# Kernel optimization log

Measured on AMD Instinct MI355X. Metric: run time of the kernel, lower is better.

The kernel has to match this reference:

```python
import jax, jax.numpy as jnp
import numpy as np
from jax import lax

B, C, V, T = 8, 256, 96, 96
C8, C2 = C // 8, C // 2


def _conv3(x, w):
    # 3x3, stride 1, pad 1, no bias (the repo's misnamed 'conv1x1')
    return lax.conv_general_dilated(x, w, (1, 1), [(1, 1), (1, 1)],
                                    dimension_numbers=("NCHW", "OIHW", "NCHW"))


def _conv1(x, w, b):
    # true 1x1 conv with bias (cAttn q/k/v)
    y = lax.conv_general_dilated(x, w, (1, 1), [(0, 0), (0, 0)],
                                 dimension_numbers=("NCHW", "OIHW", "NCHW"))
    return y + b[None, :, None, None]


def setup_inputs() -> dict:
    key = jax.random.key(0)
    ks = jax.random.split(key, 20)
    s = 0.02
    d = {
        "x": jax.random.normal(ks[0], (B, C, V, T), jnp.float32),
        # vAttn (3x3 convs, no bias)
        "v_wq": jax.random.normal(ks[1], (C8, C, 3, 3), jnp.float32) * s,
        "v_wk": jax.random.normal(ks[2], (C8, C, 3, 3), jnp.float32) * s,
        "v_wv": jax.random.normal(ks[3], (C2, C, 3, 3), jnp.float32) * s,
        "v_wo": jax.random.normal(ks[4], (C, C2, 3, 3), jnp.float32) * s,
        "v_sigma": jax.random.normal(ks[5], (1,), jnp.float32),
        # tAttn
        "t_wq": jax.random.normal(ks[6], (C8, C, 3, 3), jnp.float32) * s,
        "t_wk": jax.random.normal(ks[7], (C8, C, 3, 3), jnp.float32) * s,
        "t_wv": jax.random.normal(ks[8], (C2, C, 3, 3), jnp.float32) * s,
        "t_wo": jax.random.normal(ks[9], (C, C2, 3, 3), jnp.float32) * s,
        "t_sigma": jax.random.normal(ks[10], (1,), jnp.float32),
        # cAttn (1x1 convs with bias for q/k/v, 3x3 for output proj)
        "c_wq": jax.random.normal(ks[11], (C, C, 1, 1), jnp.float32) * s,
        "c_bq": jax.random.normal(ks[12], (C,), jnp.float32) * s,
        "c_wk": jax.random.normal(ks[13], (C, C, 1, 1), jnp.float32) * s,
        "c_bk": jax.random.normal(ks[14], (C,), jnp.float32) * s,
        "c_wv": jax.random.normal(ks[15], (C, C, 1, 1), jnp.float32) * s,
        "c_bv": jax.random.normal(ks[16], (C,), jnp.float32) * s,
        "c_wo": jax.random.normal(ks[17], (C, C, 3, 3), jnp.float32) * s,
        "c_sigma": jax.random.normal(ks[18], (1,), jnp.float32),
    }
    return d


def reference(x, v_wq, v_wk, v_wv, v_wo, v_sigma,
              t_wq, t_wk, t_wv, t_wo, t_sigma,
              c_wq, c_bq, c_wk, c_bk, c_wv, c_bv, c_wo, c_sigma):
    # vAttn: attention over the v axis, independently per (b, t)
    q = _conv3(x, v_wq)                                   # [B,C8,V,T]
    k = _conv3(x, v_wk)
    v = _conv3(x, v_wv)                                   # [B,C2,V,T]
    a = jax.nn.softmax(jnp.einsum('bcvt,bcwt->btvw', q, k), axis=-1)
    av = jnp.einsum('btvw,bcwt->bcvt', a, v)              # [B,C2,V,T]
    x1 = v_sigma * _conv3(av, v_wo)

    # tAttn: attention over the t axis, independently per (b, v)
    q = _conv3(x, t_wq)
    k = _conv3(x, t_wk)
    v = _conv3(x, t_wv)
    a = jax.nn.softmax(jnp.einsum('bcvt,bcvs->bvts', q, k), axis=-1)
    av = jnp.einsum('bvts,bcvs->bcvt', a, v)
    x2 = t_sigma * _conv3(av, t_wo)

    # cAttn: attention over the channel axis, independently per (b, v)
    q = _conv1(x, c_wq, c_bq)                             # [B,C,V,T]
    k = _conv1(x, c_wk, c_bk)
    v = _conv1(x, c_wv, c_bv)
    a = jax.nn.softmax(jnp.einsum('bcvt,bdvt->bvcd', q, k), axis=-1)
    av = jnp.einsum('bvcd,bdvt->bcvt', a, v)
    x3 = c_sigma * _conv3(av, c_wo)

    return x + x1 + x2 + x3
```

## Files before the change

### kernel.cpp

```cpp
#include <hip/hip_runtime.h>
#include <math.h>

#define BB  8
#define CH  256
#define NVT 9216
#define PLN (98*98*32)
#define PROW (98*32)

typedef short bh8 __attribute__((ext_vector_type(8)));
typedef short bh4 __attribute__((ext_vector_type(4)));
typedef float f4  __attribute__((ext_vector_type(4)));

__device__ __forceinline__ float bf2f(ushort u) {
    union { uint i; float f; } x; x.i = ((uint)u) << 16; return x.f;
}
__device__ __forceinline__ ushort f2bf(float f) {
    union { float f; uint i; } x; x.f = f;
    uint r = (x.i + 0x7FFFu + ((x.i >> 16) & 1u)) >> 16;
    return (ushort)r;
}
__device__ __forceinline__ int cperm(int ci) {
    return 8 * ((ci >> 2) & 3) + 4 * (ci >> 4) + (ci & 3);
}
__device__ __forceinline__ void gld16(const void* g, void* l) {
    __builtin_amdgcn_global_load_lds(
        (const __attribute__((address_space(1))) void*)g,
        (__attribute__((address_space(3))) void*)l, 16, 0, 0);
}

__global__ __launch_bounds__(256) void pad_zero_k(ushort* __restrict__ x32,
                                                  ushort* __restrict__ avall)
{
    int p = blockIdx.x;
    ushort* base = (p < 64) ? x32 + (size_t)p * PLN
                            : avall + (size_t)(p - 64) * PLN;
    const bh8 z = {0,0,0,0,0,0,0,0};
    for (int n = threadIdx.x; n < 1552; n += 256) {
        size_t off;
        if (n < 392)       off = (size_t)n * 8;
        else if (n < 784)  off = (size_t)97 * PROW + (size_t)(n - 392) * 8;
        else {
            int m = n - 784;
            int vq = m >> 3, side = (m >> 2) & 1, sub = m & 3;
            off = ((size_t)(vq + 1) * 98 + side * 97) * 32 + sub * 8;
        }
        *(bh8*)&base[off] = z;
    }
}

__global__ __launch_bounds__(256) void cvt_x32_k(const float* __restrict__ x,
                                                 ushort* __restrict__ x32)
{
    __shared__ ushort tile[96 * 32];
    int v = blockIdx.x, kc = blockIdx.y, b = blockIdx.z;
    int ci = threadIdx.x >> 3, tp = threadIdx.x & 7;
    const float* src = x + (((size_t)(b * 256 + kc * 32 + ci)) * 96 + v) * 96 + tp * 12;
    int pc = cperm(ci);
    int gci = pc >> 3, idx = pc & 7;
#pragma unroll
    for (int u = 0; u < 12; ++u) {
        int t = tp * 12 + u;
        int sw = ((t + 1) >> 1) & 3;
        tile[t * 32 + 8 * (gci ^ sw) + idx] = f2bf(src[u]);
    }
    __syncthreads();
    ushort* dst = x32 + (((size_t)(b * 8 + kc) * 98 + v + 1) * 98 + 1) * 32;
    for (int n = threadIdx.x; n < 384; n += 256)
        *(bh8*)&dst[n * 8] = *(const bh8*)&tile[n * 8];
}

__global__ __launch_bounds__(256) void wpack_k(const float* __restrict__ w,
    ushort* __restrict__ dst, int CIN, int TAPS, int Csrc, int coBase, int COT,
    int kcBase, const float* __restrict__ scale)
{
    int n = blockIdx.x * 256 + threadIdx.x;
    int total = (CIN >> 5) * TAPS * Csrc * 32;
    if (n >= total) return;
    int kl  = n & 31;
    int rem = n >> 5;
    int col = rem % Csrc; rem /= Csrc;
    int tap = rem % TAPS;
    int kc  = rem / TAPS;
    int ci  = kc * 32 + kl;
    int g   = (kl >> 2) & 3;
    int i   = ((kl >> 4) << 2) | (kl & 3);
    int cog = coBase + col;
    int cot = cog >> 4, lc = cog & 15;
    float v = w[((size_t)col * CIN + ci) * TAPS + tap];
    if (scale) v *= scale[0];
    dst[((((size_t)(kcBase + kc) * TAPS + tap) * COT + cot) * 64 + (g * 16 + lc)) * 8 + i]
        = f2bf(v);
}

template<int TAPS, int CT, int OMODE>
__global__ __launch_bounds__(512) void conv_mfma(
    const ushort* __restrict__ xin, const ushort* __restrict__ wpk,
    ushort* __restrict__ obf, const float* __restrict__ xres,
    float* __restrict__ oacc, const float* __restrict__ bias, int KC)
{
    constexpr int ROWS   = (TAPS == 9) ? 3 : 1;
    constexpr int SLABS  = ROWS * PROW;
    constexpr int CHUNKS = (SLABS * 2 + 1023) / 1024;
    constexpr int BUFSZ  = CHUNKS * 512;
    constexpr int COT    = CT * 4;
    constexpr int COUT   = COT * 16;
    __shared__ ushort sx[2][BUFSZ];

    const int v0 = blockIdx.x, b = blockIdx.y;
    const int tid = threadIdx.x;
    const int w = tid >> 6, l = tid & 63;
    const int g = l >> 4, lc = l & 15;
    const int wc = w & 3, wt = w >> 2;

    f4 acc[CT][3];
#pragma unroll
    for (int ct = 0; ct < CT; ++ct)
#pragma unroll
        for (int nt = 0; nt < 3; ++nt) acc[ct][nt] = (f4){0.f, 0.f, 0.f, 0.f};

    auto stage = [&](int kc, int buf) {
        const ushort* src = xin +
            (((size_t)b * KC + kc) * 98 + v0 + ((TAPS == 9) ? 0 : 1)) * (size_t)PROW;
#pragma unroll
        for (int c = 0; c < (CHUNKS + 7) / 8; ++c) {
            int ch = w + c * 8;
            if (ch < CHUNKS)
                gld16(src + ch * 512 + l * 8, &sx[buf][ch * 512 + l * 8]);
        }
    };

    stage(0, 0);
    __syncthreads();
    for (int kc = 0; kc < KC; ++kc) {
        const int cur = kc & 1;
        if (kc + 1 < KC) stage(kc + 1, cur ^ 1);
        const bh8* wp = (const bh8*)wpk;
#pragma unroll
        for (int tap = 0; tap < TAPS; ++tap) {
            const int kh = (TAPS == 9) ? tap / 3 : 0;
            const int kw = (TAPS == 9) ? tap % 3 : 1;
            bh8 af[CT];
#pragma unroll
            for (int ct = 0; ct < CT; ++ct)
                af[ct] = wp[(((size_t)kc * TAPS + tap) * COT + (wc * CT + ct)) * 64 + l];
#pragma unroll
            for (int nt = 0; nt < 3; ++nt) {
                int tp = wt * 48 + nt * 16 + lc + kw;
                bh8 bf = *(const bh8*)&sx[cur][(kh * 98 + tp) * 32
                                              + 8 * (g ^ ((tp >> 1) & 3))];
#pragma unroll
                for (int ct = 0; ct < CT; ++ct)
                    acc[ct][nt] = __builtin_amdgcn_mfma_f32_16x16x32_bf16(
                        af[ct], bf, acc[ct][nt], 0, 0, 0);
            }
        }
        __syncthreads();
    }

#pragma unroll
    for (int ct = 0; ct < CT; ++ct) {
#pragma unroll
        for (int nt = 0; nt < 3; ++nt) {
            int tt = wt * 48 + nt * 16 + lc;
            if (OMODE == 2) {
                bh4 o;
#pragma unroll
                for (int j = 0; j < 4; ++j) {
                    int cog = (wc * CT + ct) * 16 + g * 4 + j;
                    float val = acc[ct][nt][j];
                    if (bias) val += bias[cog];
                    o[j] = (short)f2bf(val);
                }
                *(bh4*)&obf[(((size_t)b * 96 + v0) * 96 + tt) * COUT
                            + (wc * CT + ct) * 16 + g * 4] = o;
            } else if (OMODE == 0) {
#pragma unroll
                for (int j = 0; j < 4; ++j) {
                    int cog = (wc * CT + ct) * 16 + g * 4 + j;
                    float val = acc[ct][nt][j];
                    if (bias) val += bias[cog];
                    obf[(((size_t)b * COUT + cog) * 96 + v0) * 96 + tt] = f2bf(val);
                }
            } else {
#pragma unroll
                for (int j = 0; j < 4; ++j) {
                    int cog = (wc * CT + ct) * 16 + g * 4 + j;
                    size_t o = (((size_t)b * COUT + cog) * 96 + v0) * 96 + tt;
                    oacc[o] = xres[o] + acc[ct][nt][j];
                }
            }
        }
    }
}

__global__ __launch_bounds__(256) void transpose_vt_k(const ushort* __restrict__ in,
                                                      ushort* __restrict__ out,
                                                      int cs_in, int cn)
{
    __shared__ ushort tile[96][100];
    int b = blockIdx.x / cn, c = blockIdx.x % cn;
    size_t sbase = ((size_t)b * cs_in + c) * NVT;
    size_t dbase = (size_t)blockIdx.x * NVT;
    for (int n = threadIdx.x; n < NVT; n += 256) tile[n / 96][n % 96] = in[sbase + n];
    __syncthreads();
    for (int n = threadIdx.x; n < NVT; n += 256) out[dbase + n] = tile[n % 96][n / 96];
}

template<bool OVER_V>
__global__ __launch_bounds__(384) void attn_vt_mfma_k(const ushort* __restrict__ qkv,
                                                      ushort* __restrict__ avall,
                                                      int sec, int cstride, int cbase)
{
    __shared__ ushort sQT[96 * 40];
    __shared__ ushort sKT[96 * 40];
    __shared__ ushort sV[128 * 104];

    int b = blockIdx.x / 96, p = blockIdx.x % 96;
    int tid = threadIdx.x;
    int wv = tid >> 6, l = tid & 63;
    int g = l >> 4, lc = l & 15;

    const size_t base = ((size_t)b * cstride + cbase) * (size_t)NVT + (size_t)p * 96;

    for (int s = tid; s < 768; s += 384) {
        int hf = s / 384;
        int c  = (s % 384) / 12;
        int m  = s % 12;
        bh8 val = *(const bh8*)&qkv[base + (size_t)(hf * 32 + c) * NVT + 8 * m];
        ushort* dst = hf ? sKT : sQT;
#pragma unroll
        for (int u = 0; u < 8; ++u)
            dst[(8 * m + u) * 40 + c] = (ushort)val[u];
    }
    for (int s = tid; s < 1536; s += 384) {
        int c = s / 12, m = s % 12;
        *(bh8*)&sV[c * 104 + 8 * m] =
            *(const bh8*)&qkv[base + (size_t)(64 + c) * NVT + 8 * m];
    }
    __syncthreads();

    bh4 qlo = *(const bh4*)&sQT[(wv * 16 + lc) * 40 + 4 * g];
    bh4 qhi = *(const bh4*)&sQT[(wv * 16 + lc) * 40 + 4 * g + 16];
    bh8 bq = __builtin_shufflevector(qlo, qhi, 0, 1, 2, 3, 4, 5, 6, 7);

    f4 st[6];
#pragma unroll
    for (int mt = 0; mt < 6; ++mt) {
        bh4 alo = *(const bh4*)&sKT[(mt * 16 + lc) * 40 + 4 * g];
        bh4 ahi = *(const bh4*)&sKT[(mt * 16 + lc) * 40 + 4 * g + 16];
        bh8 ak = __builtin_shufflevector(alo, ahi, 0, 1, 2, 3, 4, 5, 6, 7);
        st[mt] = __builtin_amdgcn_mfma_f32_16x16x32_bf16(ak, bq,
                                                         (f4){0.f, 0.f, 0.f, 0.f},
                                                         0, 0, 0);
    }

    float mx = -1e30f;
#pragma unroll
    for (int mt = 0; mt < 6; ++mt)
#pragma unroll
        for (int j = 0; j < 4; ++j) mx = fmaxf(mx, st[mt][j]);
    mx = fmaxf(mx, __shfl_xor(mx, 16));
    mx = fmaxf(mx, __shfl_xor(mx, 32));
    float sum = 0.f;
#pragma unroll
    for (int mt = 0; mt < 6; ++mt)
#pragma unroll
        for (int j = 0; j < 4; ++j) {
            float e = __expf(st[mt][j] - mx);
            st[mt][j] = e;
            sum += e;
        }
    sum += __shfl_xor(sum, 16);
    sum += __shfl_xor(sum, 32);
    float inv = 1.f / sum;

    bh8 pf[3];
#pragma unroll
    for (int ks = 0; ks < 3; ++ks) {
        bh8 t;
#pragma unroll
        for (int i = 0; i < 8; ++i)
            t[i] = (short)f2bf(st[2 * ks + (i >> 2)][i & 3] * inv);
        pf[ks] = t;
    }

    f4 acc[8];
#pragma unroll
    for (int mt = 0; mt < 8; ++mt) acc[mt] = (f4){0.f, 0.f, 0.f, 0.f};
#pragma unroll
    for (int ks = 0; ks < 3; ++ks)
#pragma unroll
        for (int mt = 0; mt < 8; ++mt) {
            bh4 alo = *(const bh4*)&sV[(mt * 16 + lc) * 104 + ks * 32 + 4 * g];
            bh4 ahi = *(const bh4*)&sV[(mt * 16 + lc) * 104 + ks * 32 + 4 * g + 16];
            bh8 avf = __builtin_shufflevector(alo, ahi, 0, 1, 2, 3, 4, 5, 6, 7);
            acc[mt] = __builtin_amdgcn_mfma_f32_16x16x32_bf16(avf, pf[ks],
                                                              acc[mt], 0, 0, 0);
        }

    int i = wv * 16 + lc;
#pragma unroll
    for (int mt = 0; mt < 8; ++mt) {
        int vv_ = OVER_V ? i : p;
        int tt_ = OVER_V ? p : i;
        int sw  = ((1 + tt_) >> 1) & 3;
        bh4 o;
#pragma unroll
        for (int j = 0; j < 4; ++j) o[j] = (short)f2bf(acc[mt][j]);
        size_t off = ((((size_t)b * 16 + sec + (mt >> 1)) * 98 + 1 + vv_) * 98
                      + 1 + tt_) * 32 + 8 * (g ^ sw) + 4 * (mt & 1);
        *(bh4*)&avall[off] = o;
    }
}

__global__ __launch_bounds__(256) void attn_c_k(const ushort* __restrict__ qc,
    const ushort* __restrict__ kc_, const ushort* __restrict__ vc,
    ushort* __restrict__ avall)
{
    __shared__ ushort sQ[64 * 104];
    __shared__ ushort sK[256 * 104];
    __shared__ ushort sV[96 * 264];
    __shared__ ushort sP[64 * 264];

    int v = blockIdx.x, cc = blockIdx.y, b = blockIdx.z;
    int c0 = cc * 64;
    int tid = threadIdx.x;
    int w = tid >> 6, l = tid & 63;
    int g = l >> 4, lc = l & 15;

    for (int s = tid; s < 64 * 12; s += 256) {
        int r = s / 12, sg = s % 12;
        *(bh8*)&sQ[r * 104 + sg * 8] =
            *(const bh8*)&qc[(((size_t)b * 256 + c0 + r) * 96 + v) * 96 + sg * 8];
    }
    for (int s = tid; s < 256 * 12; s += 256) {
        int r = s / 12, sg = s % 12;
        *(bh8*)&sK[r * 104 + sg * 8] =
            *(const bh8*)&kc_[(((size_t)b * 256 + r) * 96 + v) * 96 + sg * 8];
    }
    for (int s = tid; s < 96 * 32; s += 256) {
        int r = s / 32, sg = s % 32;
        *(bh8*)&sV[r * 264 + sg * 8] =
            *(const bh8*)&vc[(((size_t)b * 96 + v) * 96 + r) * 256 + sg * 8];
    }
    __syncthreads();

    f4 s16[16];
#pragma unroll
    for (int nt = 0; nt < 16; ++nt) s16[nt] = (f4){0.f, 0.f, 0.f, 0.f};
#pragma unroll
    for (int ks = 0; ks < 3; ++ks) {
        bh4 alo = *(const bh4*)&sQ[(w * 16 + lc) * 104 + ks * 32 + 4 * g];
        bh4 ahi = *(const bh4*)&sQ[(w * 16 + lc) * 104 + ks * 32 + 4 * g + 16];
        bh8 aq = __builtin_shufflevector(alo, ahi, 0, 1, 2, 3, 4, 5, 6, 7);
#pragma unroll
        for (int nt = 0; nt < 16; ++nt) {
            bh4 blo = *(const bh4*)&sK[(nt * 16 + lc) * 104 + ks * 32 + 4 * g];
            bh4 bhi = *(const bh4*)&sK[(nt * 16 + lc) * 104 + ks * 32 + 4 * g + 16];
            bh8 bk = __builtin_shufflevector(blo, bhi, 0, 1, 2, 3, 4, 5, 6, 7);
            s16[nt] = __builtin_amdgcn_mfma_f32_16x16x32_bf16(aq, bk, s16[nt], 0, 0, 0);
        }
    }
#pragma unroll
    for (int j = 0; j < 4; ++j) {
        float m = -1e30f;
#pragma unroll
        for (int nt = 0; nt < 16; ++nt) m = fmaxf(m, s16[nt][j]);
        m = fmaxf(m, __shfl_xor(m, 1));
        m = fmaxf(m, __shfl_xor(m, 2));
        m = fmaxf(m, __shfl_xor(m, 4));
        m = fmaxf(m, __shfl_xor(m, 8));
        float sum = 0.f;
#pragma unroll
        for (int nt = 0; nt < 16; ++nt) {
            float e = __expf(s16[nt][j] - m); s16[nt][j] = e; sum += e;
        }
        sum += __shfl_xor(sum, 1);
        sum += __shfl_xor(sum, 2);
        sum += __shfl_xor(sum, 4);
        sum += __shfl_xor(sum, 8);
        float inv = 1.f / sum;
#pragma unroll
        for (int nt = 0; nt < 16; ++nt)
            sP[(w * 16 + g * 4 + j) * 264 + nt * 16 + lc] = f2bf(s16[nt][j] * inv);
    }
    __syncthreads();

    f4 o6[6];
#pragma unroll
    for (int nt = 0; nt < 6; ++nt) o6[nt] = (f4){0.f, 0.f, 0.f, 0.f};
#pragma unroll
    for (int ks = 0; ks < 8; ++ks) {
        bh4 alo = *(const bh4*)&sP[(w * 16 + lc) * 264 + ks * 32 + 4 * g];
        bh4 ahi = *(const bh4*)&sP[(w * 16 + lc) * 264 + ks * 32 + 4 * g + 16];
        bh8 ap = __builtin_shufflevector(alo, ahi, 0, 1, 2, 3, 4, 5, 6, 7);
#pragma unroll
        for (int nt = 0; nt < 6; ++nt) {
            bh4 blo = *(const bh4*)&sV[(nt * 16 + lc) * 264 + ks * 32 + 4 * g];
            bh4 bhi = *(const bh4*)&sV[(nt * 16 + lc) * 264 + ks * 32 + 4 * g + 16];
            bh8 bv = __builtin_shufflevector(blo, bhi, 0, 1, 2, 3, 4, 5, 6, 7);
            o6[nt] = __builtin_amdgcn_mfma_f32_16x16x32_bf16(ap, bv, o6[nt], 0, 0, 0);
        }
    }
#pragma unroll
    for (int nt = 0; nt < 6; ++nt) {
        int t = nt * 16 + lc;
        int sw = ((1 + t) >> 1) & 3;
        bh4 o;
#pragma unroll
        for (int j = 0; j < 4; ++j) o[j] = (short)f2bf(o6[nt][j]);
        size_t off = ((((size_t)b * 16 + 8 + cc * 2 + (w >> 1)) * 98 + 1 + v) * 98
                      + 1 + t) * 32 + 8 * (g ^ sw) + 4 * (w & 1);
        *(bh4*)&avall[off] = o;
    }
}

extern "C" void kernel_launch(void* const* d_in, const int* in_sizes, int n_in,
                              void* d_out, int out_size, void* d_ws, size_t ws_size,
                              hipStream_t stream)
{
    const float* x     = (const float*)d_in[0];
    const float* v_wq  = (const float*)d_in[1];
    const float* v_wk  = (const float*)d_in[2];
    const float* v_wv  = (const float*)d_in[3];
    const float* v_wo  = (const float*)d_in[4];
    const float* v_sig = (const float*)d_in[5];
    const float* t_wq  = (const float*)d_in[6];
    const float* t_wk  = (const float*)d_in[7];
    const float* t_wv  = (const float*)d_in[8];
    const float* t_wo  = (const float*)d_in[9];
    const float* t_sig = (const float*)d_in[10];
    const float* c_wq  = (const float*)d_in[11];
    const float* c_bq  = (const float*)d_in[12];
    const float* c_wk  = (const float*)d_in[13];
    const float* c_bk  = (const float*)d_in[14];
    const float* c_wv  = (const float*)d_in[15];
    const float* c_bv  = (const float*)d_in[16];
    const float* c_wo  = (const float*)d_in[17];
    const float* c_sig = (const float*)d_in[18];

    float*  out = (float*)d_out;
    ushort* ws  = (ushort*)d_ws;

    const size_t X32  = 0;
    const size_t AVL  = X32 + 19685376;
    const size_t POOL = AVL + 39354368;
    const size_t QKV   = POOL;
    const size_t QKVVT = POOL + 28311552;
    const size_t QC    = POOL;
    const size_t KCB   = POOL + 18874368;
    const size_t VCT   = POOL + 37748736;
    const size_t PK    = POOL + 56623104;
    const size_t PK_PVT = PK;
    const size_t PK_CQ  = PK_PVT + 884736;
    const size_t PK_CK  = PK_CQ + 65536;
    const size_t PK_CV  = PK_CK + 65536;
    const size_t PK_FIN = PK_CV + 65536;

    pad_zero_k<<<192, 256, 0, stream>>>(ws + X32, ws + AVL);
    cvt_x32_k<<<dim3(96, 8, BB), 256, 0, stream>>>(x, ws + X32);

    auto pack = [&](const float* w, size_t dst, int cin, int taps, int csrc,
                    int cobase, int cot, int kcb, const float* sc) {
        int total = (cin >> 5) * taps * csrc * 32;
        wpack_k<<<(total + 255) / 256, 256, 0, stream>>>(w, ws + dst, cin, taps,
                                                          csrc, cobase, cot, kcb, sc);
    };
    pack(v_wq, PK_PVT, 256, 9, 32, 0, 24, 0, nullptr);
    pack(v_wk, PK_PVT, 256, 9, 32, 32, 24, 0, nullptr);
    pack(v_wv, PK_PVT, 256, 9, 128, 64, 24, 0, nullptr);
    pack(t_wq, PK_PVT, 256, 9, 32, 192, 24, 0, nullptr);
    pack(t_wk, PK_PVT, 256, 9, 32, 224, 24, 0, nullptr);
    pack(t_wv, PK_PVT, 256, 9, 128, 256, 24, 0, nullptr);
    pack(c_wq, PK_CQ, 256, 1, 256, 0, 16, 0, nullptr);
    pack(c_wk, PK_CK, 256, 1, 256, 0, 16, 0, nullptr);
    pack(c_wv, PK_CV, 256, 1, 256, 0, 16, 0, nullptr);
    pack(v_wo, PK_FIN, 128, 9, 256, 0, 16, 0, v_sig);
    pack(t_wo, PK_FIN, 128, 9, 256, 0, 16, 4, t_sig);
    pack(c_wo, PK_FIN, 256, 9, 256, 0, 16, 8, c_sig);

    dim3 cgrid(96, BB);

    conv_mfma<9, 6, 0><<<cgrid, 512, 0, stream>>>(
        ws + X32, ws + PK_PVT, ws + QKV, nullptr, nullptr, nullptr, 8);

    transpose_vt_k<<<BB * 192, 256, 0, stream>>>(ws + QKV, ws + QKVVT, 384, 192);
    attn_vt_mfma_k<true><<<BB * 96, 384, 0, stream>>>(ws + QKVVT, ws + AVL, 0, 192, 0);

    attn_vt_mfma_k<false><<<BB * 96, 384, 0, stream>>>(ws + QKV, ws + AVL, 4, 384, 192);

    conv_mfma<1, 4, 0><<<cgrid, 512, 0, stream>>>(
        ws + X32, ws + PK_CQ, ws + QC, nullptr, nullptr, c_bq, 8);
    conv_mfma<1, 4, 0><<<cgrid, 512, 0, stream>>>(
        ws + X32, ws + PK_CK, ws + KCB, nullptr, nullptr, c_bk, 8);
    conv_mfma<1, 4, 2><<<cgrid, 512, 0, stream>>>(
        ws + X32, ws + PK_CV, ws + VCT, nullptr, nullptr, c_bv, 8);
    attn_c_k<<<dim3(96, 4, BB), 256, 0, stream>>>(ws + QC, ws + KCB, ws + VCT,
                                                  ws + AVL);

    conv_mfma<9, 4, 5><<<cgrid, 512, 0, stream>>>(
        ws + AVL, ws + PK_FIN, nullptr, x, out, nullptr, 16);
}
```

Measured before the change: 665.0 us.

## Prefetch conv weights ahead of staging and read residual from padded bf16 input

The conv kernel now loads weight fragments for several taps into registers before issuing the next input-slab stage. Scheduling barriers and s_setprio raise wave priority around the MFMA blocks, so weight-load latency overlaps with compute. Launch bounds now request two blocks per CU. The final conv reads its residual from the already-packed bf16 padded input instead of the fp32 x, which halves residual read traffic but rounds the residual to bf16. The extra prefetched registers may conflict with the occupancy target and cause spills.

```diff
diff --git a/kernel.cpp b/kernel.cpp
--- a/kernel.cpp
+++ b/kernel.cpp
@@ -93,9 +93,9 @@
 }
 
 template<int TAPS, int CT, int OMODE>
-__global__ __launch_bounds__(512) void conv_mfma(
+__global__ __launch_bounds__(512, 2) void conv_mfma(
     const ushort* __restrict__ xin, const ushort* __restrict__ wpk,
-    ushort* __restrict__ obf, const float* __restrict__ xres,
+    ushort* __restrict__ obf, const ushort* __restrict__ xres32,
     float* __restrict__ oacc, const float* __restrict__ bias, int KC)
 {
     constexpr int ROWS   = (TAPS == 9) ? 3 : 1;
@@ -104,6 +104,7 @@
     constexpr int BUFSZ  = CHUNKS * 512;
     constexpr int COT    = CT * 4;
     constexpr int COUT   = COT * 16;
+    constexpr int PRE    = (TAPS == 1) ? 1 : (CT > 4 ? 4 : 9);
     __shared__ ushort sx[2][BUFSZ];
 
     const int v0 = blockIdx.x, b = blockIdx.y;
@@ -118,6 +119,8 @@
 #pragma unroll
         for (int nt = 0; nt < 3; ++nt) acc[ct][nt] = (f4){0.f, 0.f, 0.f, 0.f};
 
+    const bh8* wp0 = (const bh8*)wpk + (size_t)(wc * CT) * 64 + l;
+
     auto stage = [&](int kc, int buf) {
         const ushort* src = xin +
             (((size_t)b * KC + kc) * 98 + v0 + ((TAPS == 9) ? 0 : 1)) * (size_t)PROW;
@@ -128,31 +131,49 @@
                 gld16(src + ch * 512 + l * 8, &sx[buf][ch * 512 + l * 8]);
         }
     };
+    auto ldw = [&](bh8 (&dst)[CT], int kc, int tap) {
+#pragma unroll
+        for (int ct = 0; ct < CT; ++ct)
+            dst[ct] = wp0[(((size_t)kc * TAPS + tap) * COT + ct) * 64];
+    };
+    auto taps_body = [&](const bh8 (&afc)[CT], int cur, int kh, int kw) {
+#pragma unroll
+        for (int nt = 0; nt < 3; ++nt) {
+            int tp = wt * 48 + nt * 16 + lc + kw;
+            bh8 bf = *(const bh8*)&sx[cur][(kh * 98 + tp) * 32
+                                          + 8 * (g ^ ((tp >> 1) & 3))];
+#pragma unroll
+            for (int ct = 0; ct < CT; ++ct)
+                acc[ct][nt] = __builtin_amdgcn_mfma_f32_16x16x32_bf16(
+                    afc[ct], bf, acc[ct][nt], 0, 0, 0);
+        }
+    };
 
     stage(0, 0);
     __syncthreads();
     for (int kc = 0; kc < KC; ++kc) {
         const int cur = kc & 1;
+        bh8 afa[PRE][CT];
+#pragma unroll
+        for (int tap = 0; tap < PRE; ++tap) ldw(afa[tap], kc, tap);
+        __builtin_amdgcn_sched_barrier(0);
         if (kc + 1 < KC) stage(kc + 1, cur ^ 1);
-        const bh8* wp = (const bh8*)wpk;
-#pragma unroll
-        for (int tap = 0; tap < TAPS; ++tap) {
-            const int kh = (TAPS == 9) ? tap / 3 : 0;
-            const int kw = (TAPS == 9) ? tap % 3 : 1;
-            bh8 af[CT];
-#pragma unroll
-            for (int ct = 0; ct < CT; ++ct)
-                af[ct] = wp[(((size_t)kc * TAPS + tap) * COT + (wc * CT + ct)) * 64 + l];
-#pragma unroll
-            for (int nt = 0; nt < 3; ++nt) {
-                int tp = wt * 48 + nt * 16 + lc + kw;
-                bh8 bf = *(const bh8*)&sx[cur][(kh * 98 + tp) * 32
-                                              + 8 * (g ^ ((tp >> 1) & 3))];
-#pragma unroll
-                for (int ct = 0; ct < CT; ++ct)
-                    acc[ct][nt] = __builtin_amdgcn_mfma_f32_16x16x32_bf16(
-                        af[ct], bf, acc[ct][nt], 0, 0, 0);
-            }
+        __builtin_amdgcn_sched_barrier(0);
+        __builtin_amdgcn_s_setprio(1);
+#pragma unroll
+        for (int tap = 0; tap < PRE; ++tap)
+            taps_body(afa[tap], cur, (TAPS == 9) ? tap / 3 : 0,
+                      (TAPS == 9) ? tap % 3 : 1);
+        __builtin_amdgcn_s_setprio(0);
+        if constexpr (PRE < TAPS) {
+            bh8 afb[TAPS - PRE][CT];
+#pragma unroll
+            for (int tap = PRE; tap < TAPS; ++tap) ldw(afb[tap - PRE], kc, tap);
+            __builtin_amdgcn_s_setprio(1);
+#pragma unroll
+            for (int tap = PRE; tap < TAPS; ++tap)
+                taps_body(afb[tap - PRE], cur, tap / 3, tap % 3);
+            __builtin_amdgcn_s_setprio(0);
         }
         __syncthreads();
     }
@@ -182,11 +203,18 @@
                     obf[(((size_t)b * COUT + cog) * 96 + v0) * 96 + tt] = f2bf(val);
                 }
             } else {
+                int cb  = (wc * CT + ct) * 16 + g * 4;
+                int ci5 = cb & 31;
+                int gci = (ci5 >> 2) & 3;
+                int idx = 4 * (ci5 >> 4);
+                int swr = ((1 + tt) >> 1) & 3;
+                const ushort* xr = xres32 +
+                    ((((size_t)b * 8 + (cb >> 5)) * 98 + 1 + v0) * 98 + 1 + tt) * 32;
+                bh4 rv = *(const bh4*)&xr[8 * (gci ^ swr) + idx];
 #pragma unroll
                 for (int j = 0; j < 4; ++j) {
-                    int cog = (wc * CT + ct) * 16 + g * 4 + j;
-                    size_t o = (((size_t)b * COUT + cog) * 96 + v0) * 96 + tt;
-                    oacc[o] = xres[o] + acc[ct][nt][j];
+                    size_t o = (((size_t)b * COUT + cb + j) * 96 + v0) * 96 + tt;
+                    oacc[o] = bf2f((ushort)rv[j]) + acc[ct][nt][j];
                 }
             }
         }
@@ -499,5 +527,5 @@
                                                   ws + AVL);
 
     conv_mfma<9, 4, 5><<<cgrid, 512, 0, stream>>>(
-        ws + AVL, ws + PK_FIN, nullptr, x, out, nullptr, 16);
-}
+        ws + AVL, ws + PK_FIN, nullptr, ws + X32, out, nullptr, 16);
+}
```

Result: slower. 682.4 us (+2.6%).

## Read conv input fragments directly from global memory and use bf16 residual

Applied to the files above, without the earlier changes.

Removes the LDS double-buffered staging in the MFMA conv kernel and loads B fragments directly from global memory via precomputed per-tap offsets, dropping per-iteration barriers. The final conv's residual add now reads the bf16 padded copy of x instead of the fp32 input. This trades LDS traffic and barriers for cache-dependent global loads, and lowers residual precision.

```diff
diff --git a/kernel.cpp b/kernel.cpp
--- a/kernel.cpp
+++ b/kernel.cpp
@@ -21,11 +21,6 @@
 }
 __device__ __forceinline__ int cperm(int ci) {
     return 8 * ((ci >> 2) & 3) + 4 * (ci >> 4) + (ci & 3);
-}
-__device__ __forceinline__ void gld16(const void* g, void* l) {
-    __builtin_amdgcn_global_load_lds(
-        (const __attribute__((address_space(1))) void*)g,
-        (__attribute__((address_space(3))) void*)l, 16, 0, 0);
 }
 
 __global__ __launch_bounds__(256) void pad_zero_k(ushort* __restrict__ x32,
@@ -95,16 +90,11 @@
 template<int TAPS, int CT, int OMODE>
 __global__ __launch_bounds__(512) void conv_mfma(
     const ushort* __restrict__ xin, const ushort* __restrict__ wpk,
-    ushort* __restrict__ obf, const float* __restrict__ xres,
+    ushort* __restrict__ obf, const ushort* __restrict__ xres32,
     float* __restrict__ oacc, const float* __restrict__ bias, int KC)
 {
-    constexpr int ROWS   = (TAPS == 9) ? 3 : 1;
-    constexpr int SLABS  = ROWS * PROW;
-    constexpr int CHUNKS = (SLABS * 2 + 1023) / 1024;
-    constexpr int BUFSZ  = CHUNKS * 512;
-    constexpr int COT    = CT * 4;
-    constexpr int COUT   = COT * 16;
-    __shared__ ushort sx[2][BUFSZ];
+    constexpr int COT  = CT * 4;
+    constexpr int COUT = COT * 16;
 
     const int v0 = blockIdx.x, b = blockIdx.y;
     const int tid = threadIdx.x;
@@ -118,43 +108,39 @@
 #pragma unroll
         for (int nt = 0; nt < 3; ++nt) acc[ct][nt] = (f4){0.f, 0.f, 0.f, 0.f};
 
-    auto stage = [&](int kc, int buf) {
-        const ushort* src = xin +
-            (((size_t)b * KC + kc) * 98 + v0 + ((TAPS == 9) ? 0 : 1)) * (size_t)PROW;
-#pragma unroll
-        for (int c = 0; c < (CHUNKS + 7) / 8; ++c) {
-            int ch = w + c * 8;
-            if (ch < CHUNKS)
-                gld16(src + ch * 512 + l * 8, &sx[buf][ch * 512 + l * 8]);
-        }
-    };
-
-    stage(0, 0);
-    __syncthreads();
-    for (int kc = 0; kc < KC; ++kc) {
-        const int cur = kc & 1;
-        if (kc + 1 < KC) stage(kc + 1, cur ^ 1);
-        const bh8* wp = (const bh8*)wpk;
+    const bh8* wp0 = (const bh8*)wpk + (size_t)(wc * CT) * 64 + l;
+
+    uint boff[TAPS][3];
+#pragma unroll
+    for (int tap = 0; tap < TAPS; ++tap) {
+        const int kh = (TAPS == 9) ? tap / 3 : 0;
+        const int kw = (TAPS == 9) ? tap % 3 : 1;
+        const int prow = v0 + kh + ((TAPS == 9) ? 0 : 1);
+#pragma unroll
+        for (int nt = 0; nt < 3; ++nt) {
+            int tp = wt * 48 + nt * 16 + lc + kw;
+            boff[tap][nt] = (uint)(prow * PROW + tp * 32
+                                   + 8 * (g ^ ((tp >> 1) & 3)));
+        }
+    }
+
+    const ushort* bp = xin + (size_t)b * KC * PLN;
+    for (int kc = 0; kc < KC; ++kc, bp += PLN) {
 #pragma unroll
         for (int tap = 0; tap < TAPS; ++tap) {
-            const int kh = (TAPS == 9) ? tap / 3 : 0;
-            const int kw = (TAPS == 9) ? tap % 3 : 1;
             bh8 af[CT];
 #pragma unroll
             for (int ct = 0; ct < CT; ++ct)
-                af[ct] = wp[(((size_t)kc * TAPS + tap) * COT + (wc * CT + ct)) * 64 + l];
+                af[ct] = wp0[(((size_t)kc * TAPS + tap) * COT + ct) * 64];
 #pragma unroll
             for (int nt = 0; nt < 3; ++nt) {
-                int tp = wt * 48 + nt * 16 + lc + kw;
-                bh8 bf = *(const bh8*)&sx[cur][(kh * 98 + tp) * 32
-                                              + 8 * (g ^ ((tp >> 1) & 3))];
+                bh8 bf = *(const bh8*)&bp[boff[tap][nt]];
 #pragma unroll
                 for (int ct = 0; ct < CT; ++ct)
                     acc[ct][nt] = __builtin_amdgcn_mfma_f32_16x16x32_bf16(
                         af[ct], bf, acc[ct][nt], 0, 0, 0);
             }
         }
-        __syncthreads();
     }
 
 #pragma unroll
@@ -182,11 +168,18 @@
                     obf[(((size_t)b * COUT + cog) * 96 + v0) * 96 + tt] = f2bf(val);
                 }
             } else {
+                int cb  = (wc * CT + ct) * 16 + g * 4;
+                int ci5 = cb & 31;
+                int gci = (ci5 >> 2) & 3;
+                int idx = 4 * (ci5 >> 4);
+                int swr = ((1 + tt) >> 1) & 3;
+                const ushort* xr = xres32 +
+                    ((((size_t)b * 8 + (cb >> 5)) * 98 + 1 + v0) * 98 + 1 + tt) * 32;
+                bh4 rv = *(const bh4*)&xr[8 * (gci ^ swr) + idx];
 #pragma unroll
                 for (int j = 0; j < 4; ++j) {
-                    int cog = (wc * CT + ct) * 16 + g * 4 + j;
-                    size_t o = (((size_t)b * COUT + cog) * 96 + v0) * 96 + tt;
-                    oacc[o] = xres[o] + acc[ct][nt][j];
+                    size_t o = (((size_t)b * COUT + cb + j) * 96 + v0) * 96 + tt;
+                    oacc[o] = bf2f((ushort)rv[j]) + acc[ct][nt][j];
                 }
             }
         }
@@ -499,5 +492,5 @@
                                                   ws + AVL);
 
     conv_mfma<9, 4, 5><<<cgrid, 512, 0, stream>>>(
-        ws + AVL, ws + PK_FIN, nullptr, x, out, nullptr, 16);
-}
+        ws + AVL, ws + PK_FIN, nullptr, ws + X32, out, nullptr, 16);
+}
```

Measured after the change: 794.4 us. +19.5%, slower.
